# Kernel tuning notes

Hardware: AMD Instinct MI355X
Metric: run time of the kernel (lower is better)

## Reference

```python
import jax, jax.numpy as jnp
import numpy as np

N, E, IN_CH, EDGE_DIM, OUT_CH = 50000, 600000, 128, 64, 128


def setup_inputs() -> dict:
    key = jax.random.key(0)
    ks = jax.random.split(key, 9)
    return {
        "x": jax.random.normal(ks[0], (N, IN_CH), dtype=jnp.float32),
        "edge_index": jax.random.randint(ks[1], (2, E), 0, N, dtype=jnp.int64),
        "edge_attr": jax.random.normal(ks[2], (E, EDGE_DIM), dtype=jnp.float32),
        "Wx": jax.random.normal(ks[3], (IN_CH, OUT_CH), dtype=jnp.float32) * 0.05,
        "bx": jax.random.normal(ks[4], (OUT_CH,), dtype=jnp.float32) * 0.05,
        "We": jax.random.normal(ks[5], (EDGE_DIM, OUT_CH), dtype=jnp.float32) * 0.05,
        "be": jax.random.normal(ks[6], (OUT_CH,), dtype=jnp.float32) * 0.05,
        "Wm": jax.random.normal(ks[7], (2 * OUT_CH, OUT_CH), dtype=jnp.float32) * 0.05,
        "bm": jax.random.normal(ks[8], (OUT_CH,), dtype=jnp.float32) * 0.05,
        "beta": jnp.float32(0.1),
    }


def reference(x, edge_index, edge_attr, Wx, bx, We, be, Wm, bm, beta):
    # node / edge projections
    xp = x @ Wx + bx                      # [N, out]
    ef = edge_attr @ We + be              # [E, out]
    src, dst = edge_index[0], edge_index[1]
    # gather source node features, combine with edge features
    msg = jnp.concatenate([xp[src], ef], axis=1)   # [E, 2*out]
    msg = jax.nn.leaky_relu(msg @ Wm + bm)         # slope 0.01 matches torch default
    # scatter-add into destination nodes
    agg = jax.ops.segment_sum(msg, dst, num_segments=xp.shape[0])  # [N, out]
    return jax.nn.sigmoid(agg) * jax.nn.relu(beta)
```

## Files before the change

kernel.cpp:

```cpp
#include <hip/hip_runtime.h>


#define NB 25000
#define NB_SHIFT 1
#define TPW 4

typedef __bf16 bf16x8 __attribute__((ext_vector_type(8)));
typedef float  f32x4  __attribute__((ext_vector_type(4)));
typedef unsigned short ushort_t;
typedef unsigned int   uint_t;

__device__ __forceinline__ ushort_t f2b(float f) {
    uint_t u = __float_as_uint(f);
    u += 0x7FFF + ((u >> 16) & 1);
    return (ushort_t)(u >> 16);
}
__device__ __forceinline__ uint_t pack2(float a, float b) {
    return (uint_t)f2b(a) | ((uint_t)f2b(b) << 16);
}

__global__ void fuse_weights_kernel(const float* __restrict__ Wx,
                                    const float* __restrict__ bx,
                                    const float* __restrict__ We,
                                    const float* __restrict__ be,
                                    const float* __restrict__ Wm,
                                    const float* __restrict__ bm,
                                    ushort_t* __restrict__ WxmT16,
                                    ushort_t* __restrict__ WemT16,
                                    float* __restrict__ bf) {
    int idx = blockIdx.x * blockDim.x + threadIdx.x;
    if (idx < 128 * 128) {
        int r = idx >> 7, c = idx & 127;
        float acc = 0.f;
        #pragma unroll 8
        for (int j = 0; j < 128; ++j) acc += Wx[r * 128 + j] * Wm[j * 128 + c];
        WxmT16[c * 128 + r] = f2b(acc);
    } else if (idx < 128 * 128 + 64 * 128) {
        int t = idx - 128 * 128;
        int r = t >> 7, c = t & 127;
        float acc = 0.f;
        #pragma unroll 8
        for (int j = 0; j < 128; ++j) acc += We[r * 128 + j] * Wm[(128 + j) * 128 + c];
        WemT16[c * 64 + r] = f2b(acc);
    } else if (idx < 128 * 128 + 64 * 128 + 128) {
        int c = idx - (128 * 128 + 64 * 128);
        float acc = bm[c];
        #pragma unroll 8
        for (int j = 0; j < 128; ++j)
            acc += bx[j] * Wm[j * 128 + c] + be[j] * Wm[(128 + j) * 128 + c];
        bf[c] = acc;
    }
}

__global__ __launch_bounds__(256) void node_gemm_kernel(
        const float* __restrict__ x, const ushort_t* __restrict__ WxmT16,
        const float* __restrict__ bf, ushort_t* __restrict__ ub, int N) {
    int tid = threadIdx.x;
    int g = blockIdx.x * 4 + (tid >> 6);
    if (g >= (N / 16) * 2) return;
    int lane = tid & 63, l15 = lane & 15, quad = lane >> 4;
    int n0 = (g >> 1) * 16;
    int chBase = (g & 1) * 64;

    bf16x8 B[4][4];
    #pragma unroll
    for (int ct = 0; ct < 4; ++ct)
        #pragma unroll
        for (int kk = 0; kk < 4; ++kk)
            B[ct][kk] = __builtin_bit_cast(bf16x8, *((const uint4*)
                &WxmT16[(size_t)(chBase + ct * 16 + l15) * 128 + kk * 32 + quad * 8]));

    bf16x8 A[4];
    #pragma unroll
    for (int kk = 0; kk < 4; ++kk) {
        const float4* s = (const float4*)&x[(size_t)(n0 + l15) * 128 + kk * 32 + quad * 8];
        float4 v0 = s[0], v1 = s[1];
        uint4 w;
        w.x = pack2(v0.x, v0.y);
        w.y = pack2(v0.z, v0.w);
        w.z = pack2(v1.x, v1.y);
        w.w = pack2(v1.z, v1.w);
        A[kk] = __builtin_bit_cast(bf16x8, w);
    }

    f32x4 acc[4] = {{0.f,0.f,0.f,0.f},{0.f,0.f,0.f,0.f},
                    {0.f,0.f,0.f,0.f},{0.f,0.f,0.f,0.f}};
    #pragma unroll
    for (int kk = 0; kk < 4; ++kk)
        #pragma unroll
        for (int ct = 0; ct < 4; ++ct)
            acc[ct] = __builtin_amdgcn_mfma_f32_16x16x32_bf16(B[ct][kk], A[kk], acc[ct], 0, 0, 0);

    #pragma unroll
    for (int ct = 0; ct < 4; ++ct) {
        int ch = chBase + ct * 16 + quad * 4;
        float4 bv = *(const float4*)&bf[ch];
        uint2 w;
        w.x = pack2(acc[ct][0] + bv.x, acc[ct][1] + bv.y);
        w.y = pack2(acc[ct][2] + bv.z, acc[ct][3] + bv.w);
        *((uint2*)&ub[(size_t)(n0 + l15) * 128 + ch]) = w;
    }
}

__global__ __launch_bounds__(256) void hist_kernel(
        const int* __restrict__ ei, int* __restrict__ cnt, int E) {
    int e = blockIdx.x * 256 + threadIdx.x;
    if (e < E) atomicAdd(&cnt[ei[E + e] >> NB_SHIFT], 1);
}

__global__ __launch_bounds__(1024) void scan_kernel(
        const int* __restrict__ cnt, int* __restrict__ start,
        int* __restrict__ cur, int nb, int E) {
    __shared__ int tot[1024];
    int t = threadIdx.x;
    int v[25]; int sum = 0;
    #pragma unroll
    for (int j = 0; j < 25; ++j) {
        int i = t * 25 + j;
        v[j] = (i < nb) ? cnt[i] : 0;
        sum += v[j];
    }
    tot[t] = sum;
    __syncthreads();
    for (int d = 1; d < 1024; d <<= 1) {
        int val = tot[t];
        int add = (t >= d) ? tot[t - d] : 0;
        __syncthreads();
        tot[t] = val + add;
        __syncthreads();
    }
    int ex = (t == 0) ? 0 : tot[t - 1];
    #pragma unroll
    for (int j = 0; j < 25; ++j) {
        int i = t * 25 + j;
        if (i < nb) { start[i] = ex; cur[i] = ex; }
        ex += v[j];
    }
    if (t == 1023) start[nb] = ex;
}

__global__ __launch_bounds__(256) void binpos_kernel(
        const int* __restrict__ ei, int* __restrict__ cur,
        uint2* __restrict__ rec64, int E) {
    int e = blockIdx.x * 256 + threadIdx.x;
    if (e >= E) return;
    int d = ei[E + e];
    int b = d >> NB_SHIFT;
    int p = atomicAdd(&cur[b], 1);
    uint_t src  = (uint_t)ei[e];
    uint_t dstl = (uint_t)(d & ((1 << NB_SHIFT) - 1));
    uint2 r;
    r.x = src | (dstl << 16);
    r.y = (uint_t)e;
    rec64[p] = r;
}

__global__ __launch_bounds__(256) void msg_stream_kernel(
        const float* __restrict__ ea,
        const ushort_t* __restrict__ WemT16, ushort_t* __restrict__ msgl, int E) {
    int tid = threadIdx.x;
    int g = blockIdx.x * 4 + (tid >> 6);
    int grp = g >> 1;
    int chBase = (g & 1) << 6;
    int t0 = grp * (TPW * 16);
    if (t0 >= E) return;
    int lane = tid & 63, l15 = lane & 15, quad = lane >> 4;

    bf16x8 B[4][2];
    #pragma unroll
    for (int ct = 0; ct < 4; ++ct)
        #pragma unroll
        for (int kk = 0; kk < 2; ++kk)
            B[ct][kk] = __builtin_bit_cast(bf16x8, *((const uint4*)
                &WemT16[(size_t)(chBase + ct * 16 + l15) * 64 + kk * 32 + quad * 8]));

    if (t0 + TPW * 16 <= E) {
        bf16x8 a0[TPW], a1[TPW];
        #pragma unroll
        for (int tt = 0; tt < TPW; ++tt) {
            int t16 = t0 + tt * 16;
            const float* rowp = &ea[(size_t)(t16 + l15) * 64];
            const float4* sA = (const float4*)(rowp + quad * 8);
            float4 v0 = sA[0], v1 = sA[1];
            uint4 w0;
            w0.x = pack2(v0.x, v0.y);
            w0.y = pack2(v0.z, v0.w);
            w0.z = pack2(v1.x, v1.y);
            w0.w = pack2(v1.z, v1.w);
            a0[tt] = __builtin_bit_cast(bf16x8, w0);
            const float4* sB = (const float4*)(rowp + 32 + quad * 8);
            float4 v2 = sB[0], v3 = sB[1];
            uint4 w1;
            w1.x = pack2(v2.x, v2.y);
            w1.y = pack2(v2.z, v2.w);
            w1.z = pack2(v3.x, v3.y);
            w1.w = pack2(v3.z, v3.w);
            a1[tt] = __builtin_bit_cast(bf16x8, w1);
        }
        #pragma unroll
        for (int tt = 0; tt < TPW; ++tt) {
            int t16 = t0 + tt * 16;
            f32x4 acc[4] = {{0.f,0.f,0.f,0.f},{0.f,0.f,0.f,0.f},
                            {0.f,0.f,0.f,0.f},{0.f,0.f,0.f,0.f}};
            #pragma unroll
            for (int ct = 0; ct < 4; ++ct)
                acc[ct] = __builtin_amdgcn_mfma_f32_16x16x32_bf16(B[ct][0], a0[tt], acc[ct], 0, 0, 0);
            #pragma unroll
            for (int ct = 0; ct < 4; ++ct)
                acc[ct] = __builtin_amdgcn_mfma_f32_16x16x32_bf16(B[ct][1], a1[tt], acc[ct], 0, 0, 0);
            #pragma unroll
            for (int ct = 0; ct < 4; ++ct) {
                uint2 w;
                w.x = pack2(acc[ct][0], acc[ct][1]);
                w.y = pack2(acc[ct][2], acc[ct][3]);
                *((uint2*)&msgl[(size_t)(t16 + l15) * 128 + chBase + ct * 16 + quad * 4]) = w;
            }
        }
    } else {
        for (int tt = 0; tt < TPW; ++tt) {
            int t16 = t0 + tt * 16;
            if (t16 >= E) break;
            const float* rowp = &ea[(size_t)(t16 + l15) * 64];
            const float4* sA = (const float4*)(rowp + quad * 8);
            float4 v0 = sA[0], v1 = sA[1];
            uint4 w0;
            w0.x = pack2(v0.x, v0.y);
            w0.y = pack2(v0.z, v0.w);
            w0.z = pack2(v1.x, v1.y);
            w0.w = pack2(v1.z, v1.w);
            bf16x8 a0 = __builtin_bit_cast(bf16x8, w0);
            const float4* sB = (const float4*)(rowp + 32 + quad * 8);
            float4 v2 = sB[0], v3 = sB[1];
            uint4 w1;
            w1.x = pack2(v2.x, v2.y);
            w1.y = pack2(v2.z, v2.w);
            w1.z = pack2(v3.x, v3.y);
            w1.w = pack2(v3.z, v3.w);
            bf16x8 a1 = __builtin_bit_cast(bf16x8, w1);

            f32x4 acc[4] = {{0.f,0.f,0.f,0.f},{0.f,0.f,0.f,0.f},
                            {0.f,0.f,0.f,0.f},{0.f,0.f,0.f,0.f}};
            #pragma unroll
            for (int ct = 0; ct < 4; ++ct)
                acc[ct] = __builtin_amdgcn_mfma_f32_16x16x32_bf16(B[ct][0], a0, acc[ct], 0, 0, 0);
            #pragma unroll
            for (int ct = 0; ct < 4; ++ct)
                acc[ct] = __builtin_amdgcn_mfma_f32_16x16x32_bf16(B[ct][1], a1, acc[ct], 0, 0, 0);
            #pragma unroll
            for (int ct = 0; ct < 4; ++ct) {
                uint2 w;
                w.x = pack2(acc[ct][0], acc[ct][1]);
                w.y = pack2(acc[ct][2], acc[ct][3]);
                *((uint2*)&msgl[(size_t)(t16 + l15) * 128 + chBase + ct * 16 + quad * 4]) = w;
            }
        }
    }
}

__global__ __launch_bounds__(256) void segsum_kernel(
        const ushort_t* __restrict__ msgl, const ushort_t* __restrict__ ub,
        const uint2* __restrict__ rec64, const int* __restrict__ start,
        const float* __restrict__ beta, float* __restrict__ out, int N) {
    int wid = blockIdx.x * 4 + (threadIdx.x >> 6);
    if (wid >= NB) return;
    int lane = threadIdx.x & 63;
    int q = lane >> 4;
    int c16 = lane & 15;

    int s0 = start[wid], s1 = start[wid + 1];
    float a0[8] = {0.f,0.f,0.f,0.f,0.f,0.f,0.f,0.f};
    float a1[8] = {0.f,0.f,0.f,0.f,0.f,0.f,0.f,0.f};

    uint2 zero; zero.x = 0u; zero.y = 0u;
    int pA = s0 + q;
    uint2 rA = (pA < s1) ? rec64[pA] : zero;
    int pB = pA + 4;
    uint2 rB = (pB < s1) ? rec64[pB] : zero;

    uint4 mvA = *(const uint4*)&msgl[(size_t)rA.y * 128 + (c16 << 3)];
    uint4 uvA = *(const uint4*)&ub[(size_t)(rA.x & 0xFFFFu) * 128 + (c16 << 3)];

    while (pA < s1) {
        int pC = pB + 4;
        uint2 rC = (pC < s1) ? rec64[pC] : zero;
        uint4 mvB = *(const uint4*)&msgl[(size_t)rB.y * 128 + (c16 << 3)];
        uint4 uvB = *(const uint4*)&ub[(size_t)(rB.x & 0xFFFFu) * 128 + (c16 << 3)];

        float w1 = (rA.x >> 16) ? 1.f : 0.f;
        float w0 = 1.f - w1;
        {
            float mlo, mhi;
            mlo = __uint_as_float(mvA.x << 16)         + __uint_as_float(uvA.x << 16);
            mhi = __uint_as_float(mvA.x & 0xFFFF0000u) + __uint_as_float(uvA.x & 0xFFFF0000u);
            mlo = fmaxf(mlo, 0.01f * mlo); mhi = fmaxf(mhi, 0.01f * mhi);
            a0[0] += mlo * w0; a1[0] += mlo * w1;
            a0[1] += mhi * w0; a1[1] += mhi * w1;
            mlo = __uint_as_float(mvA.y << 16)         + __uint_as_float(uvA.y << 16);
            mhi = __uint_as_float(mvA.y & 0xFFFF0000u) + __uint_as_float(uvA.y & 0xFFFF0000u);
            mlo = fmaxf(mlo, 0.01f * mlo); mhi = fmaxf(mhi, 0.01f * mhi);
            a0[2] += mlo * w0; a1[2] += mlo * w1;
            a0[3] += mhi * w0; a1[3] += mhi * w1;
            mlo = __uint_as_float(mvA.z << 16)         + __uint_as_float(uvA.z << 16);
            mhi = __uint_as_float(mvA.z & 0xFFFF0000u) + __uint_as_float(uvA.z & 0xFFFF0000u);
            mlo = fmaxf(mlo, 0.01f * mlo); mhi = fmaxf(mhi, 0.01f * mhi);
            a0[4] += mlo * w0; a1[4] += mlo * w1;
            a0[5] += mhi * w0; a1[5] += mhi * w1;
            mlo = __uint_as_float(mvA.w << 16)         + __uint_as_float(uvA.w << 16);
            mhi = __uint_as_float(mvA.w & 0xFFFF0000u) + __uint_as_float(uvA.w & 0xFFFF0000u);
            mlo = fmaxf(mlo, 0.01f * mlo); mhi = fmaxf(mhi, 0.01f * mhi);
            a0[6] += mlo * w0; a1[6] += mlo * w1;
            a0[7] += mhi * w0; a1[7] += mhi * w1;
        }

        pA = pB; rA = rB; mvA = mvB; uvA = uvB;
        pB = pC; rB = rC;
    }

    #pragma unroll
    for (int j = 0; j < 8; ++j) {
        a0[j] += __shfl_xor(a0[j], 16);
        a0[j] += __shfl_xor(a0[j], 32);
        a1[j] += __shfl_xor(a1[j], 16);
        a1[j] += __shfl_xor(a1[j], 32);
    }

    float rb = beta[0];
    rb = rb > 0.f ? rb : 0.f;
    int h   = lane >> 5;
    int sub = (lane >> 4) & 1;
    int n = (wid << 1) + h;
    if (n < N) {
        float x0, x1, x2, x3;
        if (h == 0) {
            if (sub == 0) { x0 = a0[0]; x1 = a0[1]; x2 = a0[2]; x3 = a0[3]; }
            else          { x0 = a0[4]; x1 = a0[5]; x2 = a0[6]; x3 = a0[7]; }
        } else {
            if (sub == 0) { x0 = a1[0]; x1 = a1[1]; x2 = a1[2]; x3 = a1[3]; }
            else          { x0 = a1[4]; x1 = a1[5]; x2 = a1[6]; x3 = a1[7]; }
        }
        float4 v;
        v.x = rb / (1.f + __expf(-x0));
        v.y = rb / (1.f + __expf(-x1));
        v.z = rb / (1.f + __expf(-x2));
        v.w = rb / (1.f + __expf(-x3));
        ((float4*)out)[(size_t)n * 32 + c16 * 2 + sub] = v;
    }
}

extern "C" void kernel_launch(void* const* d_in, const int* in_sizes, int n_in,
                              void* d_out, int out_size, void* d_ws, size_t ws_size,
                              hipStream_t stream) {
    const float* x    = (const float*)d_in[0];
    const int*   ei   = (const int*)d_in[1];
    const float* ea   = (const float*)d_in[2];
    const float* Wx   = (const float*)d_in[3];
    const float* bx   = (const float*)d_in[4];
    const float* We   = (const float*)d_in[5];
    const float* be   = (const float*)d_in[6];
    const float* Wm   = (const float*)d_in[7];
    const float* bm   = (const float*)d_in[8];
    const float* beta = (const float*)d_in[9];

    int N = in_sizes[0] / 128;
    int E = in_sizes[2] / 64;

    float* out = (float*)d_out;

    char* ws = (char*)d_ws;
    ushort_t* WxmT16 = (ushort_t*)(ws);
    ushort_t* WemT16 = (ushort_t*)(ws + 32768);
    float*    bf     = (float*)(ws + 49152);
    ushort_t* ub     = (ushort_t*)(ws + 65536);
    size_t off = 65536 + (size_t)N * 128 * 2;
    uint2* rec64   = (uint2*)(ws + off);
    off += (size_t)E * 8;
    int* cnt       = (int*)(ws + off);
    int* startb    = (int*)(ws + off + 131072);
    int* cur       = (int*)(ws + off + 262144);
    ushort_t* msgl = (ushort_t*)(ws + off + 393216);

    hipMemsetAsync(cnt, 0, (size_t)NB * sizeof(int), stream);

    fuse_weights_kernel<<<(24704 + 255) / 256, 256, 0, stream>>>(
        Wx, bx, We, be, Wm, bm, WxmT16, WemT16, bf);

    node_gemm_kernel<<<(N / 16 * 2 + 3) / 4, 256, 0, stream>>>(
        x, WxmT16, bf, ub, N);

    int ebBlocks = (E + 255) / 256;
    hist_kernel<<<ebBlocks, 256, 0, stream>>>(ei, cnt, E);
    scan_kernel<<<1, 1024, 0, stream>>>(cnt, startb, cur, NB, E);
    binpos_kernel<<<ebBlocks, 256, 0, stream>>>(ei, cur, rec64, E);

    int ntile  = (E + 15) / 16;
    int ngrp   = (ntile + TPW - 1) / TPW;
    int nwaves = ngrp * 2;
    msg_stream_kernel<<<(nwaves + 3) / 4, 256, 0, stream>>>(
        ea, WemT16, msgl, E);

    segsum_kernel<<<(NB + 3) / 4, 256, 0, stream>>>(
        msgl, ub, rec64, startb, beta, out, N);
}
```

Baseline: 475.7 us.

## Fuse edge message GEMM with scatter-add using LDS atomics over sorted edges

```diff
diff --git a/kernel.cpp b/kernel.cpp
--- a/kernel.cpp
+++ b/kernel.cpp
@@ -3,7 +3,8 @@
 
 #define NB 25000
 #define NB_SHIFT 1
-#define TPW 4
+#define EPB 64
+#define LSLOT 32
 
 typedef __bf16 bf16x8 __attribute__((ext_vector_type(8)));
 typedef float  f32x4  __attribute__((ext_vector_type(4)));
@@ -17,6 +18,9 @@
 }
 __device__ __forceinline__ uint_t pack2(float a, float b) {
     return (uint_t)f2b(a) | ((uint_t)f2b(b) << 16);
+}
+__device__ __forceinline__ float b2f(ushort_t v) {
+    return __uint_as_float((uint_t)v << 16);
 }
 
 __global__ void fuse_weights_kernel(const float* __restrict__ Wx,
@@ -109,8 +113,7 @@
 }
 
 __global__ __launch_bounds__(1024) void scan_kernel(
-        const int* __restrict__ cnt, int* __restrict__ start,
-        int* __restrict__ cur, int nb, int E) {
+        const int* __restrict__ cnt, int* __restrict__ cur, int nb) {
     __shared__ int tot[1024];
     int t = threadIdx.x;
     int v[25]; int sum = 0;
@@ -133,10 +136,9 @@
     #pragma unroll
     for (int j = 0; j < 25; ++j) {
         int i = t * 25 + j;
-        if (i < nb) { start[i] = ex; cur[i] = ex; }
+        if (i < nb) cur[i] = ex;
         ex += v[j];
     }
-    if (t == 1023) start[nb] = ex;
 }
 
 __global__ __launch_bounds__(256) void binpos_kernel(
@@ -147,24 +149,27 @@
     int d = ei[E + e];
     int b = d >> NB_SHIFT;
     int p = atomicAdd(&cur[b], 1);
-    uint_t src  = (uint_t)ei[e];
-    uint_t dstl = (uint_t)(d & ((1 << NB_SHIFT) - 1));
     uint2 r;
-    r.x = src | (dstl << 16);
-    r.y = (uint_t)e;
+    r.x = (uint_t)e;
+    r.y = (uint_t)ei[e] | ((uint_t)d << 16);
     rec64[p] = r;
 }
 
-__global__ __launch_bounds__(256) void msg_stream_kernel(
-        const float* __restrict__ ea,
-        const ushort_t* __restrict__ WemT16, ushort_t* __restrict__ msgl, int E) {
+__global__ __launch_bounds__(256) void edge_fused_kernel(
+        const float* __restrict__ ea, const uint2* __restrict__ rec64,
+        const ushort_t* __restrict__ WemT16, const ushort_t* __restrict__ ub,
+        float* __restrict__ agg, int E) {
+    __shared__ float accum[LSLOT * 132];
+
     int tid = threadIdx.x;
-    int g = blockIdx.x * 4 + (tid >> 6);
-    int grp = g >> 1;
-    int chBase = (g & 1) << 6;
-    int t0 = grp * (TPW * 16);
-    if (t0 >= E) return;
-    int lane = tid & 63, l15 = lane & 15, quad = lane >> 4;
+    int p0 = blockIdx.x * EPB;
+    int p1 = p0 + EPB; if (p1 > E) p1 = E;
+
+    for (int i = tid; i < LSLOT * 132; i += 256) accum[i] = 0.f;
+
+    int w = tid >> 6, lane = tid & 63;
+    int l15 = lane & 15, quad = lane >> 4;
+    int chBase = (w & 1) << 6;
 
     bf16x8 B[4][2];
     #pragma unroll
@@ -174,177 +179,93 @@
             B[ct][kk] = __builtin_bit_cast(bf16x8, *((const uint4*)
                 &WemT16[(size_t)(chBase + ct * 16 + l15) * 64 + kk * 32 + quad * 8]));
 
-    if (t0 + TPW * 16 <= E) {
-        bf16x8 a0[TPW], a1[TPW];
-        #pragma unroll
-        for (int tt = 0; tt < TPW; ++tt) {
-            int t16 = t0 + tt * 16;
-            const float* rowp = &ea[(size_t)(t16 + l15) * 64];
-            const float4* sA = (const float4*)(rowp + quad * 8);
-            float4 v0 = sA[0], v1 = sA[1];
-            uint4 w0;
-            w0.x = pack2(v0.x, v0.y);
-            w0.y = pack2(v0.z, v0.w);
-            w0.z = pack2(v1.x, v1.y);
-            w0.w = pack2(v1.z, v1.w);
-            a0[tt] = __builtin_bit_cast(bf16x8, w0);
-            const float4* sB = (const float4*)(rowp + 32 + quad * 8);
-            float4 v2 = sB[0], v3 = sB[1];
-            uint4 w1;
-            w1.x = pack2(v2.x, v2.y);
-            w1.y = pack2(v2.z, v2.w);
-            w1.z = pack2(v3.x, v3.y);
-            w1.w = pack2(v3.z, v3.w);
-            a1[tt] = __builtin_bit_cast(bf16x8, w1);
-        }
-        #pragma unroll
-        for (int tt = 0; tt < TPW; ++tt) {
-            int t16 = t0 + tt * 16;
-            f32x4 acc[4] = {{0.f,0.f,0.f,0.f},{0.f,0.f,0.f,0.f},
-                            {0.f,0.f,0.f,0.f},{0.f,0.f,0.f,0.f}};
-            #pragma unroll
-            for (int ct = 0; ct < 4; ++ct)
-                acc[ct] = __builtin_amdgcn_mfma_f32_16x16x32_bf16(B[ct][0], a0[tt], acc[ct], 0, 0, 0);
-            #pragma unroll
-            for (int ct = 0; ct < 4; ++ct)
-                acc[ct] = __builtin_amdgcn_mfma_f32_16x16x32_bf16(B[ct][1], a1[tt], acc[ct], 0, 0, 0);
+    int node_lo = (int)(rec64[p0].y >> 16) & ~1;
+
+    __syncthreads();
+
+    #pragma unroll
+    for (int ui = 0; ui < 2; ++ui) {
+        int tile = (w >> 1) + ui * 2;
+        int pt = p0 + tile * 16;
+        if (pt >= E) continue;
+
+        int p = pt + l15;
+        uint2 rec = rec64[p < E ? p : (E - 1)];
+
+        const float* rowp = &ea[(size_t)rec.x * 64];
+        const float4* sA = (const float4*)(rowp + quad * 8);
+        float4 v0 = sA[0], v1 = sA[1];
+        const float4* sB = (const float4*)(rowp + 32 + quad * 8);
+        float4 v2 = sB[0], v3 = sB[1];
+        uint4 w0, w1;
+        w0.x = pack2(v0.x, v0.y);
+        w0.y = pack2(v0.z, v0.w);
+        w0.z = pack2(v1.x, v1.y);
+        w0.w = pack2(v1.z, v1.w);
+        w1.x = pack2(v2.x, v2.y);
+        w1.y = pack2(v2.z, v2.w);
+        w1.z = pack2(v3.x, v3.y);
+        w1.w = pack2(v3.z, v3.w);
+        bf16x8 a0 = __builtin_bit_cast(bf16x8, w0);
+        bf16x8 a1 = __builtin_bit_cast(bf16x8, w1);
+
+        f32x4 acc[4] = {{0.f,0.f,0.f,0.f},{0.f,0.f,0.f,0.f},
+                        {0.f,0.f,0.f,0.f},{0.f,0.f,0.f,0.f}};
+        #pragma unroll
+        for (int ct = 0; ct < 4; ++ct)
+            acc[ct] = __builtin_amdgcn_mfma_f32_16x16x32_bf16(a0, B[ct][0], acc[ct], 0, 0, 0);
+        #pragma unroll
+        for (int ct = 0; ct < 4; ++ct)
+            acc[ct] = __builtin_amdgcn_mfma_f32_16x16x32_bf16(a1, B[ct][1], acc[ct], 0, 0, 0);
+
+        int me = E - pt;
+        #pragma unroll
+        for (int r = 0; r < 4; ++r) {
+            int mm = quad * 4 + r;
+            uint_t ry = __shfl(rec.y, mm);
+            int sr = (int)(ry & 0xFFFFu);
+            int dst = (int)(ry >> 16);
+            int nl = dst - node_lo;
+            bool vm = mm < me;
             #pragma unroll
             for (int ct = 0; ct < 4; ++ct) {
-                uint2 w;
-                w.x = pack2(acc[ct][0], acc[ct][1]);
-                w.y = pack2(acc[ct][2], acc[ct][3]);
-                *((uint2*)&msgl[(size_t)(t16 + l15) * 128 + chBase + ct * 16 + quad * 4]) = w;
+                int ch = chBase + ct * 16 + l15;
+                float m = acc[ct][r] + b2f(ub[(size_t)sr * 128 + ch]);
+                m = fmaxf(m, 0.01f * m);
+                if (vm) {
+                    if (nl < LSLOT)
+                        atomicAdd(&accum[nl * 132 + ch], m);
+                    else
+                        atomicAdd(&agg[(size_t)dst * 128 + ch], m);
+                }
             }
         }
-    } else {
-        for (int tt = 0; tt < TPW; ++tt) {
-            int t16 = t0 + tt * 16;
-            if (t16 >= E) break;
-            const float* rowp = &ea[(size_t)(t16 + l15) * 64];
-            const float4* sA = (const float4*)(rowp + quad * 8);
-            float4 v0 = sA[0], v1 = sA[1];
-            uint4 w0;
-            w0.x = pack2(v0.x, v0.y);
-            w0.y = pack2(v0.z, v0.w);
-            w0.z = pack2(v1.x, v1.y);
-            w0.w = pack2(v1.z, v1.w);
-            bf16x8 a0 = __builtin_bit_cast(bf16x8, w0);
-            const float4* sB = (const float4*)(rowp + 32 + quad * 8);
-            float4 v2 = sB[0], v3 = sB[1];
-            uint4 w1;
-            w1.x = pack2(v2.x, v2.y);
-            w1.y = pack2(v2.z, v2.w);
-            w1.z = pack2(v3.x, v3.y);
-            w1.w = pack2(v3.z, v3.w);
-            bf16x8 a1 = __builtin_bit_cast(bf16x8, w1);
-
-            f32x4 acc[4] = {{0.f,0.f,0.f,0.f},{0.f,0.f,0.f,0.f},
-                            {0.f,0.f,0.f,0.f},{0.f,0.f,0.f,0.f}};
-            #pragma unroll
-            for (int ct = 0; ct < 4; ++ct)
-                acc[ct] = __builtin_amdgcn_mfma_f32_16x16x32_bf16(B[ct][0], a0, acc[ct], 0, 0, 0);
-            #pragma unroll
-            for (int ct = 0; ct < 4; ++ct)
-                acc[ct] = __builtin_amdgcn_mfma_f32_16x16x32_bf16(B[ct][1], a1, acc[ct], 0, 0, 0);
-            #pragma unroll
-            for (int ct = 0; ct < 4; ++ct) {
-                uint2 w;
-                w.x = pack2(acc[ct][0], acc[ct][1]);
-                w.y = pack2(acc[ct][2], acc[ct][3]);
-                *((uint2*)&msgl[(size_t)(t16 + l15) * 128 + chBase + ct * 16 + quad * 4]) = w;
-            }
-        }
-    }
-}
-
-__global__ __launch_bounds__(256) void segsum_kernel(
-        const ushort_t* __restrict__ msgl, const ushort_t* __restrict__ ub,
-        const uint2* __restrict__ rec64, const int* __restrict__ start,
-        const float* __restrict__ beta, float* __restrict__ out, int N) {
-    int wid = blockIdx.x * 4 + (threadIdx.x >> 6);
-    if (wid >= NB) return;
-    int lane = threadIdx.x & 63;
-    int q = lane >> 4;
-    int c16 = lane & 15;
-
-    int s0 = start[wid], s1 = start[wid + 1];
-    float a0[8] = {0.f,0.f,0.f,0.f,0.f,0.f,0.f,0.f};
-    float a1[8] = {0.f,0.f,0.f,0.f,0.f,0.f,0.f,0.f};
-
-    uint2 zero; zero.x = 0u; zero.y = 0u;
-    int pA = s0 + q;
-    uint2 rA = (pA < s1) ? rec64[pA] : zero;
-    int pB = pA + 4;
-    uint2 rB = (pB < s1) ? rec64[pB] : zero;
-
-    uint4 mvA = *(const uint4*)&msgl[(size_t)rA.y * 128 + (c16 << 3)];
-    uint4 uvA = *(const uint4*)&ub[(size_t)(rA.x & 0xFFFFu) * 128 + (c16 << 3)];
-
-    while (pA < s1) {
-        int pC = pB + 4;
-        uint2 rC = (pC < s1) ? rec64[pC] : zero;
-        uint4 mvB = *(const uint4*)&msgl[(size_t)rB.y * 128 + (c16 << 3)];
-        uint4 uvB = *(const uint4*)&ub[(size_t)(rB.x & 0xFFFFu) * 128 + (c16 << 3)];
-
-        float w1 = (rA.x >> 16) ? 1.f : 0.f;
-        float w0 = 1.f - w1;
-        {
-            float mlo, mhi;
-            mlo = __uint_as_float(mvA.x << 16)         + __uint_as_float(uvA.x << 16);
-            mhi = __uint_as_float(mvA.x & 0xFFFF0000u) + __uint_as_float(uvA.x & 0xFFFF0000u);
-            mlo = fmaxf(mlo, 0.01f * mlo); mhi = fmaxf(mhi, 0.01f * mhi);
-            a0[0] += mlo * w0; a1[0] += mlo * w1;
-            a0[1] += mhi * w0; a1[1] += mhi * w1;
-            mlo = __uint_as_float(mvA.y << 16)         + __uint_as_float(uvA.y << 16);
-            mhi = __uint_as_float(mvA.y & 0xFFFF0000u) + __uint_as_float(uvA.y & 0xFFFF0000u);
-            mlo = fmaxf(mlo, 0.01f * mlo); mhi = fmaxf(mhi, 0.01f * mhi);
-            a0[2] += mlo * w0; a1[2] += mlo * w1;
-            a0[3] += mhi * w0; a1[3] += mhi * w1;
-            mlo = __uint_as_float(mvA.z << 16)         + __uint_as_float(uvA.z << 16);
-            mhi = __uint_as_float(mvA.z & 0xFFFF0000u) + __uint_as_float(uvA.z & 0xFFFF0000u);
-            mlo = fmaxf(mlo, 0.01f * mlo); mhi = fmaxf(mhi, 0.01f * mhi);
-            a0[4] += mlo * w0; a1[4] += mlo * w1;
-            a0[5] += mhi * w0; a1[5] += mhi * w1;
-            mlo = __uint_as_float(mvA.w << 16)         + __uint_as_float(uvA.w << 16);
-            mhi = __uint_as_float(mvA.w & 0xFFFF0000u) + __uint_as_float(uvA.w & 0xFFFF0000u);
-            mlo = fmaxf(mlo, 0.01f * mlo); mhi = fmaxf(mhi, 0.01f * mhi);
-            a0[6] += mlo * w0; a1[6] += mlo * w1;
-            a0[7] += mhi * w0; a1[7] += mhi * w1;
-        }
-
-        pA = pB; rA = rB; mvA = mvB; uvA = uvB;
-        pB = pC; rB = rC;
-    }
-
-    #pragma unroll
-    for (int j = 0; j < 8; ++j) {
-        a0[j] += __shfl_xor(a0[j], 16);
-        a0[j] += __shfl_xor(a0[j], 32);
-        a1[j] += __shfl_xor(a1[j], 16);
-        a1[j] += __shfl_xor(a1[j], 32);
-    }
-
+    }
+    __syncthreads();
+
+    int node_hi = ((int)(rec64[p1 - 1].y >> 16)) | 1;
+    int span = node_hi - node_lo + 1;
+    if (span > LSLOT) span = LSLOT;
+    for (int i = tid; i < span * 128; i += 256) {
+        int nl = i >> 7, c = i & 127;
+        float v = accum[nl * 132 + c];
+        if (v != 0.f) atomicAdd(&agg[(size_t)(node_lo + nl) * 128 + c], v);
+    }
+}
+
+__global__ __launch_bounds__(256) void finalize_kernel(
+        const float* __restrict__ agg, const float* __restrict__ beta,
+        float* __restrict__ out, int n4) {
+    int gid = blockIdx.x * 256 + threadIdx.x;
+    if (gid >= n4) return;
     float rb = beta[0];
     rb = rb > 0.f ? rb : 0.f;
-    int h   = lane >> 5;
-    int sub = (lane >> 4) & 1;
-    int n = (wid << 1) + h;
-    if (n < N) {
-        float x0, x1, x2, x3;
-        if (h == 0) {
-            if (sub == 0) { x0 = a0[0]; x1 = a0[1]; x2 = a0[2]; x3 = a0[3]; }
-            else          { x0 = a0[4]; x1 = a0[5]; x2 = a0[6]; x3 = a0[7]; }
-        } else {
-            if (sub == 0) { x0 = a1[0]; x1 = a1[1]; x2 = a1[2]; x3 = a1[3]; }
-            else          { x0 = a1[4]; x1 = a1[5]; x2 = a1[6]; x3 = a1[7]; }
-        }
-        float4 v;
-        v.x = rb / (1.f + __expf(-x0));
-        v.y = rb / (1.f + __expf(-x1));
-        v.z = rb / (1.f + __expf(-x2));
-        v.w = rb / (1.f + __expf(-x3));
-        ((float4*)out)[(size_t)n * 32 + c16 * 2 + sub] = v;
-    }
+    float4 v = ((const float4*)agg)[gid];
+    v.x = rb / (1.f + __expf(-v.x));
+    v.y = rb / (1.f + __expf(-v.y));
+    v.z = rb / (1.f + __expf(-v.z));
+    v.w = rb / (1.f + __expf(-v.w));
+    ((float4*)out)[gid] = v;
 }
 
 extern "C" void kernel_launch(void* const* d_in, const int* in_sizes, int n_in,
@@ -375,11 +296,11 @@
     uint2* rec64   = (uint2*)(ws + off);
     off += (size_t)E * 8;
     int* cnt       = (int*)(ws + off);
-    int* startb    = (int*)(ws + off + 131072);
-    int* cur       = (int*)(ws + off + 262144);
-    ushort_t* msgl = (ushort_t*)(ws + off + 393216);
+    int* cur       = (int*)(ws + off + 131072);
+    float* agg     = (float*)(ws + off + 262144);
 
     hipMemsetAsync(cnt, 0, (size_t)NB * sizeof(int), stream);
+    hipMemsetAsync(agg, 0, (size_t)N * 128 * sizeof(float), stream);
 
     fuse_weights_kernel<<<(24704 + 255) / 256, 256, 0, stream>>>(
         Wx, bx, We, be, Wm, bm, WxmT16, WemT16, bf);
@@ -389,15 +310,13 @@
 
     int ebBlocks = (E + 255) / 256;
     hist_kernel<<<ebBlocks, 256, 0, stream>>>(ei, cnt, E);
-    scan_kernel<<<1, 1024, 0, stream>>>(cnt, startb, cur, NB, E);
+    scan_kernel<<<1, 1024, 0, stream>>>(cnt, cur, NB);
     binpos_kernel<<<ebBlocks, 256, 0, stream>>>(ei, cur, rec64, E);
 
-    int ntile  = (E + 15) / 16;
-    int ngrp   = (ntile + TPW - 1) / TPW;
-    int nwaves = ngrp * 2;
-    msg_stream_kernel<<<(nwaves + 3) / 4, 256, 0, stream>>>(
-        ea, WemT16, msgl, E);
-
-    segsum_kernel<<<(NB + 3) / 4, 256, 0, stream>>>(
-        msgl, ub, rec64, startb, beta, out, N);
-}
+    int fBlocks = (E + EPB - 1) / EPB;
+    edge_fused_kernel<<<fBlocks, 256, 0, stream>>>(
+        ea, rec64, WemT16, ub, agg, E);
+
+    int n4 = N * 32;
+    finalize_kernel<<<(n4 + 255) / 256, 256, 0, stream>>>(agg, beta, out, n4);
+}
```

After: 743.2 us. 1.56x slower.
